# Kernel optimization log

Measured on AMD Instinct MI355X. Metric: run time of the kernel, lower is better.

## Reference

```python
import jax, jax.numpy as jnp
import numpy as np

D_MODEL = 1024
N_HEADS = 16
D_K = D_MODEL // N_HEADS


def setup_inputs() -> dict:
    key = jax.random.key(0)
    kx, kq, kk, kv, ko = jax.random.split(key, 5)
    scale = 1.0 / np.sqrt(D_MODEL)
    return {
        "x": jax.random.normal(kx, (2, 2048, D_MODEL), dtype=jnp.float32),
        "W_Q": jax.random.normal(kq, (D_MODEL, D_MODEL), dtype=jnp.float32) * scale,
        "W_K": jax.random.normal(kk, (D_MODEL, D_MODEL), dtype=jnp.float32) * scale,
        "W_V": jax.random.normal(kv, (D_MODEL, D_MODEL), dtype=jnp.float32) * scale,
        "W_O": jax.random.normal(ko, (D_MODEL, D_MODEL), dtype=jnp.float32) * scale,
    }


def reference(x, W_Q, W_K, W_V, W_O) -> jnp.ndarray:
    B, S, _ = x.shape
    # Projections; weights stored as (d_model, d_model), applied as x @ W (Linear weight transposed convention folded into init)
    def heads(w):
        return jnp.einsum('bsd,de->bse', x, w).reshape(B, S, N_HEADS, D_K).transpose(0, 2, 1, 3)
    Q, K, V = heads(W_Q), heads(W_K), heads(W_V)  # (B,H,S,d_k)
    scores = jnp.einsum('bhqd,bhkd->bhqk', Q, K) / jnp.sqrt(jnp.asarray(D_K, x.dtype))
    causal_mask = jnp.triu(jnp.ones((S, S), dtype=bool), k=1)  # True above diagonal
    scores = jnp.where(causal_mask[None, None], jnp.asarray(-jnp.inf, x.dtype), scores)
    attn = jax.nn.softmax(scores, axis=-1)
    out = jnp.einsum('bhqk,bhkd->bhqd', attn, V)  # (B,H,S,d_k)
    out = out.transpose(0, 2, 1, 3).reshape(B, S, N_HEADS * D_K)
    return jnp.einsum('bsd,de->bse', out, W_O)
```

## Files before the change

### kernel.cpp

```cpp
#include <hip/hip_runtime.h>

typedef unsigned short u16;
typedef unsigned int u32;
typedef __attribute__((ext_vector_type(8))) __bf16 bf16x8;
typedef __attribute__((ext_vector_type(2))) __bf16 bf16x2;
typedef __attribute__((ext_vector_type(4))) float f32x4;
typedef __attribute__((ext_vector_type(16))) float f32x16;
typedef __attribute__((ext_vector_type(4))) u32 u32x4;

__device__ inline u16 f2bf(float f) {
  unsigned u = __builtin_bit_cast(unsigned, f);
  u += 0x7FFFu + ((u >> 16) & 1u);
  return (u16)(u >> 16);
}

__device__ inline u32 packbf(float a, float b) {
  bf16x2 t;
  t[0] = (__bf16)a;
  t[1] = (__bf16)b;
  return __builtin_bit_cast(u32, t);
}

__device__ inline void async16(const void* g, void* l) {
  __builtin_amdgcn_global_load_lds((const __attribute__((address_space(1))) void*)g,
                                   (__attribute__((address_space(3))) void*)l, 16, 0, 0);
}

__global__ __launch_bounds__(256) void xconv(const float* __restrict__ x, u16* __restrict__ xb) {
  int i = blockIdx.x * 256 + threadIdx.x;
  float4 v = ((const float4*)x)[i];
  ushort4 r;
  r.x = f2bf(v.x); r.y = f2bf(v.y); r.z = f2bf(v.z); r.w = f2bf(v.w);
  ((ushort4*)xb)[i] = r;
}

__global__ __launch_bounds__(256) void wtrans4(const float* __restrict__ W0,
                                               const float* __restrict__ W1,
                                               const float* __restrict__ W2,
                                               const float* __restrict__ W3,
                                               u16* __restrict__ WtQKV,
                                               u16* __restrict__ WtO) {
  __shared__ u16 tile[32][33];
  const int z = blockIdx.z;
  const float* W = (z == 0) ? W0 : (z == 1) ? W1 : (z == 2) ? W2 : W3;
  u16* Wt = (z < 3) ? (WtQKV + (size_t)z * 1024 * 1024) : WtO;
  const float s = (z == 0) ? 0.18033688011112042f : 1.0f;
  const int e0 = blockIdx.x * 32;
  const int d0 = blockIdx.y * 32;
  const int tx = threadIdx.x & 31;
  const int ty = threadIdx.x >> 5;
#pragma unroll
  for (int i = ty; i < 32; i += 8)
    tile[i][tx] = f2bf(W[(size_t)(d0 + i) * 1024 + e0 + tx] * s);
  __syncthreads();
#pragma unroll
  for (int i = ty; i < 32; i += 8)
    Wt[(size_t)(e0 + i) * 1024 + d0 + tx] = tile[tx][i];
}

__global__ __launch_bounds__(256) void vtrans(const u16* __restrict__ QKV, u16* __restrict__ Vtg) {
  __shared__ u16 t[32][66];
  const int tid = threadIdx.x;
  const int s0 = blockIdx.x * 32, dg0 = blockIdx.y * 64, b = blockIdx.z;
  {
    const int i = tid >> 3, c = (tid & 7) * 8;
    uint4 v = *(const uint4*)(QKV + (size_t)(b * 2048 + s0 + i) * 3072 + 2048 + dg0 + c);
    u16 tmp[8];
    *(uint4*)tmp = v;
#pragma unroll
    for (int e = 0; e < 8; ++e) t[i][c + e] = tmp[e];
  }
  __syncthreads();
  {
    const int r = tid >> 2, cg = (tid & 3) * 8;
    u16 tmp[8];
#pragma unroll
    for (int e = 0; e < 8; ++e) {
      const int x = cg + e;
      const int sx = (x & ~12) | ((x & 4) << 1) | ((x & 8) >> 1);
      tmp[e] = t[sx][r];
    }
    *(uint4*)(Vtg + (size_t)(b * 1024 + dg0 + r) * 2048 + s0 + cg) = *(uint4*)tmp;
  }
}

template <int OUT_BF16>
__global__ __launch_bounds__(256) void gemm_bt(const u16* __restrict__ A,
                                               const u16* __restrict__ Bt,
                                               void* __restrict__ Cp,
                                               int M, int N, int K) {
  __shared__ __align__(16) u16 As[128 * 32];
  __shared__ __align__(16) u16 Bs[128 * 32];
  const int tid = threadIdx.x;
  const int lane = tid & 63;
  const int wave = tid >> 6;
  const int lr = lane & 15;
  const int lk = (lane >> 4) * 8;
  const int wm = (wave >> 1) * 64;
  const int wn = (wave & 1) * 64;
  const int bm = blockIdx.x * 128;
  const int bn = blockIdx.y * 128;
  const int srow = lane >> 2;
  const int scol = (lane & 3) * 8;

  f32x4 acc[4][4] = {};

  for (int k0 = 0; k0 < K; k0 += 32) {
#pragma unroll
    for (int r = 0; r < 2; ++r) {
      const int chunk = r * 4 + wave;
      const int row = chunk * 16 + srow;
      async16(A + (size_t)(bm + row) * K + k0 + scol, &As[chunk * 512 + lane * 8]);
      async16(Bt + (size_t)(bn + row) * K + k0 + scol, &Bs[chunk * 512 + lane * 8]);
    }
    __syncthreads();
    bf16x8 a[4], b[4];
#pragma unroll
    for (int i = 0; i < 4; ++i) {
      a[i] = *(const bf16x8*)&As[(wm + i * 16 + lr) * 32 + lk];
      b[i] = *(const bf16x8*)&Bs[(wn + i * 16 + lr) * 32 + lk];
    }
#pragma unroll
    for (int mi = 0; mi < 4; ++mi)
#pragma unroll
      for (int ni = 0; ni < 4; ++ni)
        acc[mi][ni] = __builtin_amdgcn_mfma_f32_16x16x32_bf16(a[mi], b[ni], acc[mi][ni], 0, 0, 0);
    __syncthreads();
  }

#pragma unroll
  for (int mi = 0; mi < 4; ++mi) {
#pragma unroll
    for (int ni = 0; ni < 4; ++ni) {
      const int col = bn + wn + ni * 16 + lr;
#pragma unroll
      for (int j = 0; j < 4; ++j) {
        const int row = bm + wm + mi * 16 + (lane >> 4) * 4 + j;
        if (OUT_BF16)
          ((u16*)Cp)[(size_t)row * N + col] = f2bf(acc[mi][ni][j]);
        else
          ((float*)Cp)[(size_t)row * N + col] = acc[mi][ni][j];
      }
    }
  }
}

__global__ __launch_bounds__(256, 2) void attn_kernel(const u16* __restrict__ QKV,
                                                      const u16* __restrict__ Vtg,
                                                      u16* __restrict__ Opart,
                                                      float* __restrict__ Lpart) {
  constexpr int S = 2048, LD = 3072;
  constexpr float MFIX = 12.0f;
  __shared__ __align__(16) u16 Ks[2][64 * 64];
  __shared__ __align__(16) u16 Vs[2][64 * 64];

  const int g = 7 - (blockIdx.x >> 1);
  const int c = blockIdx.x & 1;
  const int bh = blockIdx.y;
  const int b = bh >> 4, h = bh & 15;
  const int tid = threadIdx.x, lane = tid & 63, w = tid >> 6;
  const int l31 = lane & 31, lh = lane >> 5;

  const int qbase = g * 256 + w * 64;
  const int ktlast = 4 * g + w;
  const int ktbeg = c * (2 * g + 2);
  const int ktend = (c + 1) * (2 * g + 2);

  bf16x8 qf[2][4];
#pragma unroll
  for (int qh = 0; qh < 2; ++qh) {
    const u16* qrow = QKV + (size_t)(b * S + qbase + qh * 32 + l31) * LD + h * 64;
#pragma unroll
    for (int cc = 0; cc < 4; ++cc) qf[qh][cc] = *(const bf16x8*)(qrow + cc * 16 + lh * 8);
  }

  const int c0 = tid, c1 = tid + 256;
  const int r0 = c0 >> 3, x0 = ((c0 & 7) ^ (r0 & 7)) << 3;
  const int r1 = c1 >> 3, x1 = ((c1 & 7) ^ (r1 & 7)) << 3;
  const u16* Kbase = QKV + (size_t)b * S * LD + 1024 + h * 64;
  const u16* Vbase = Vtg + (size_t)bh * 64 * 2048;

#define STAGE(buf, kt_)                                                          \
  do {                                                                           \
    async16(Kbase + (size_t)((kt_)*64 + r0) * LD + x0, &Ks[buf][c0 * 8]);        \
    async16(Kbase + (size_t)((kt_)*64 + r1) * LD + x1, &Ks[buf][c1 * 8]);        \
    async16(Vbase + (size_t)r0 * 2048 + (kt_)*64 + x0, &Vs[buf][c0 * 8]);        \
    async16(Vbase + (size_t)r1 * 2048 + (kt_)*64 + x1, &Vs[buf][c1 * 8]);        \
  } while (0)

  f32x16 o00 = {}, o01 = {}, o10 = {}, o11 = {};
  float l0 = 0.f, l1 = 0.f;

#define TREE16(dst, arr)                                                         \
  do {                                                                           \
    float v_[16];                                                                \
    _Pragma("unroll") for (int r_ = 0; r_ < 16; ++r_) v_[r_] = (arr)[r_];        \
    _Pragma("unroll") for (int s_ = 8; s_ >= 1; s_ >>= 1)                        \
      _Pragma("unroll") for (int r_ = 0; r_ < s_; ++r_) v_[r_] += v_[r_ + s_];   \
    dst += v_[0];                                                                \
  } while (0)

#define MAKE_PA(pa, pk, q4)                                                      \
  bf16x8 pa;                                                                     \
  {                                                                              \
    u32x4 wv_;                                                                   \
    wv_[0] = (pk)[(q4) + 0];                                                     \
    wv_[1] = (pk)[(q4) + 1];                                                     \
    wv_[2] = (pk)[(q4) + 2];                                                     \
    wv_[3] = (pk)[(q4) + 3];                                                     \
    pa = __builtin_bit_cast(bf16x8, wv_);                                        \
  }

  STAGE(0, ktbeg);

  int cur = 0;
  for (int kt = ktbeg; kt < ktend; ++kt) {
    if (kt + 1 < ktend) {
      STAGE(cur ^ 1, kt + 1);
      asm volatile("s_waitcnt vmcnt(4)" ::: "memory");
    } else {
      asm volatile("s_waitcnt vmcnt(0)" ::: "memory");
    }
    __builtin_amdgcn_s_barrier();
    __builtin_amdgcn_sched_barrier(0);

    const bool active = (kt <= ktlast);
    if (active) {
      const bool full = (kt < ktlast);
      const u16* ks = Ks[cur];
      const u16* vs = Vs[cur];

      f32x16 t00 = {}, t10 = {}, t01 = {}, t11 = {};
      __builtin_amdgcn_s_setprio(1);
#pragma unroll
      for (int cc = 0; cc < 4; ++cc) {
        const int ci = 2 * cc + lh;
        const bf16x8 kf0 = *(const bf16x8*)&ks[l31 * 64 + ((ci ^ (l31 & 7)) << 3)];
        const bf16x8 kf1 = *(const bf16x8*)&ks[(32 + l31) * 64 + ((ci ^ (l31 & 7)) << 3)];
        t00 = __builtin_amdgcn_mfma_f32_32x32x16_bf16(kf0, qf[0][cc], t00, 0, 0, 0);
        t01 = __builtin_amdgcn_mfma_f32_32x32x16_bf16(kf0, qf[1][cc], t01, 0, 0, 0);
        if (full) t10 = __builtin_amdgcn_mfma_f32_32x32x16_bf16(kf1, qf[0][cc], t10, 0, 0, 0);
        t11 = __builtin_amdgcn_mfma_f32_32x32x16_bf16(kf1, qf[1][cc], t11, 0, 0, 0);
      }
      __builtin_amdgcn_s_setprio(0);

      if (!full) {
#pragma unroll
        for (int r = 0; r < 16; ++r) {
          const int ko = (r & 3) + 8 * (r >> 2) + 4 * lh;
          if (ko > l31) { t00[r] = -3e38f; t11[r] = -3e38f; }
        }
      }

      u32 pk0[8], pk1[8];

#pragma unroll
      for (int r = 0; r < 16; ++r) t00[r] = exp2f(t00[r] - MFIX);
#pragma unroll
      for (int r = 0; r < 16; ++r) t01[r] = exp2f(t01[r] - MFIX);
      TREE16(l0, t00);
      TREE16(l1, t01);
#pragma unroll
      for (int j = 0; j < 8; ++j) {
        pk0[j] = packbf(t00[2 * j], t00[2 * j + 1]);
        pk1[j] = packbf(t01[2 * j], t01[2 * j + 1]);
      }
      __builtin_amdgcn_s_setprio(1);
#pragma unroll
      for (int kc = 0; kc < 2; ++kc) {
        const int q4 = kc * 4;
        MAKE_PA(pa0, pk0, q4)
        MAKE_PA(pa1, pk1, q4)
        const int ci = 2 * kc + lh;
        const bf16x8 vd0 = *(const bf16x8*)&vs[l31 * 64 + ((ci ^ (l31 & 7)) << 3)];
        const bf16x8 vd1 = *(const bf16x8*)&vs[(32 + l31) * 64 + ((ci ^ (l31 & 7)) << 3)];
        o00 = __builtin_amdgcn_mfma_f32_32x32x16_bf16(pa0, vd0, o00, 0, 0, 0);
        o01 = __builtin_amdgcn_mfma_f32_32x32x16_bf16(pa0, vd1, o01, 0, 0, 0);
        o10 = __builtin_amdgcn_mfma_f32_32x32x16_bf16(pa1, vd0, o10, 0, 0, 0);
        o11 = __builtin_amdgcn_mfma_f32_32x32x16_bf16(pa1, vd1, o11, 0, 0, 0);
      }
      __builtin_amdgcn_s_setprio(0);

      if (full) {
#pragma unroll
        for (int r = 0; r < 16; ++r) t10[r] = exp2f(t10[r] - MFIX);
        TREE16(l0, t10);
#pragma unroll
        for (int j = 0; j < 8; ++j) pk0[j] = packbf(t10[2 * j], t10[2 * j + 1]);
      }
#pragma unroll
      for (int r = 0; r < 16; ++r) t11[r] = exp2f(t11[r] - MFIX);
      TREE16(l1, t11);
#pragma unroll
      for (int j = 0; j < 8; ++j) pk1[j] = packbf(t11[2 * j], t11[2 * j + 1]);

      __builtin_amdgcn_s_setprio(1);
#pragma unroll
      for (int kc = 0; kc < 2; ++kc) {
        const int q4 = kc * 4;
        MAKE_PA(pa1, pk1, q4)
        const int ci = 2 * (kc + 2) + lh;
        const bf16x8 vd0 = *(const bf16x8*)&vs[l31 * 64 + ((ci ^ (l31 & 7)) << 3)];
        const bf16x8 vd1 = *(const bf16x8*)&vs[(32 + l31) * 64 + ((ci ^ (l31 & 7)) << 3)];
        if (full) {
          MAKE_PA(pa0, pk0, q4)
          o00 = __builtin_amdgcn_mfma_f32_32x32x16_bf16(pa0, vd0, o00, 0, 0, 0);
          o01 = __builtin_amdgcn_mfma_f32_32x32x16_bf16(pa0, vd1, o01, 0, 0, 0);
        }
        o10 = __builtin_amdgcn_mfma_f32_32x32x16_bf16(pa1, vd0, o10, 0, 0, 0);
        o11 = __builtin_amdgcn_mfma_f32_32x32x16_bf16(pa1, vd1, o11, 0, 0, 0);
      }
      __builtin_amdgcn_s_setprio(0);
    }

    asm volatile("s_waitcnt lgkmcnt(0)" ::: "memory");
    __builtin_amdgcn_s_barrier();
    cur ^= 1;
  }
#undef STAGE
#undef TREE16
#undef MAKE_PA

  const float l0t = l0 + __shfl_xor(l0, 32);
  const float l1t = l1 + __shfl_xor(l1, 32);
  u16* Oc = Opart + (size_t)c * 4096 * 1024;
#pragma unroll
  for (int r = 0; r < 16; ++r) {
    const int qo = (r & 3) + 8 * (r >> 2) + 4 * lh;
    u16* p0 = Oc + (size_t)(b * S + qbase + qo) * 1024 + h * 64 + l31;
    u16* p1 = p0 + (size_t)32 * 1024;
    p0[0] = f2bf(o00[r]);
    p0[32] = f2bf(o01[r]);
    p1[0] = f2bf(o10[r]);
    p1[32] = f2bf(o11[r]);
  }
  if (lh == 0) {
    Lpart[(size_t)c * 4096 * 16 + (size_t)(b * S + qbase + l31) * 16 + h] = l0t;
    Lpart[(size_t)c * 4096 * 16 + (size_t)(b * S + qbase + 32 + l31) * 16 + h] = l1t;
  }
}

__global__ __launch_bounds__(256) void combine(const u16* __restrict__ Opart,
                                               const float* __restrict__ Lpart,
                                               u16* __restrict__ Obuf) {
  const int i = blockIdx.x * 256 + threadIdx.x;
  const int row = i >> 7;
  const int cw = (i & 127) * 8;
  const int h = cw >> 6;
  const float l = Lpart[(size_t)row * 16 + h] + Lpart[(size_t)4096 * 16 + (size_t)row * 16 + h];
  const float inv = 1.0f / l;
  const bf16x8 a = *(const bf16x8*)(Opart + (size_t)row * 1024 + cw);
  const bf16x8 bq = *(const bf16x8*)(Opart + (size_t)4096 * 1024 + (size_t)row * 1024 + cw);
  u16 out[8];
#pragma unroll
  for (int j = 0; j < 8; ++j) out[j] = f2bf(((float)a[j] + (float)bq[j]) * inv);
  *(uint4*)(Obuf + (size_t)row * 1024 + cw) = *(uint4*)out;
}

extern "C" void kernel_launch(void* const* d_in, const int* in_sizes, int n_in,
                              void* d_out, int out_size, void* d_ws, size_t ws_size,
                              hipStream_t stream) {
  const float* x  = (const float*)d_in[0];
  const float* WQ = (const float*)d_in[1];
  const float* WK = (const float*)d_in[2];
  const float* WV = (const float*)d_in[3];
  const float* WO = (const float*)d_in[4];
  float* out = (float*)d_out;

  u16* xb    = (u16*)d_ws;
  u16* WtQKV = xb + (size_t)4096 * 1024;
  u16* WtO   = WtQKV + (size_t)3072 * 1024;
  u16* QKV   = WtO + (size_t)1024 * 1024;
  u16* Obuf  = QKV + (size_t)4096 * 3072;
  u16* Vtg   = Obuf + (size_t)4096 * 1024;
  u16* Opart = Vtg + (size_t)2048 * 2048;
  float* Lpart = (float*)(Opart + (size_t)2 * 4096 * 1024);

  xconv<<<4096, 256, 0, stream>>>(x, xb);
  wtrans4<<<dim3(32, 32, 4), 256, 0, stream>>>(WQ, WK, WV, WO, WtQKV, WtO);

  gemm_bt<1><<<dim3(32, 24), 256, 0, stream>>>(xb, WtQKV, QKV, 4096, 3072, 1024);
  vtrans<<<dim3(64, 16, 2), 256, 0, stream>>>(QKV, Vtg);
  attn_kernel<<<dim3(16, 32), 256, 0, stream>>>(QKV, Vtg, Opart, Lpart);
  combine<<<2048, 256, 0, stream>>>(Opart, Lpart, Obuf);
  gemm_bt<0><<<dim3(32, 8), 256, 0, stream>>>(Obuf, WtO, out, 4096, 1024, 1024);
}
```

Before: 140.6 us.

## Use 128-key attention tiles and merge input-conversion launches into one prep kernel

The attention kernel now stages 128-key K/V tiles per iteration instead of 64, halving the number of barrier and wait steps per block. Each tile is processed as four 32-key sub-blocks with per-wave causal masking on the diagonal. Separately, the x conversion and the weight transposes are fused into a single launch using an extra grid z-slice. Larger tiles double LDS use per block, which may lower occupancy under the two-blocks-per-CU launch bound, and they coarsen the split of work on the causal diagonal.

```diff
diff --git a/kernel.cpp b/kernel.cpp
--- a/kernel.cpp
+++ b/kernel.cpp
@@ -26,22 +26,27 @@
                                    (__attribute__((address_space(3))) void*)l, 16, 0, 0);
 }
 
-__global__ __launch_bounds__(256) void xconv(const float* __restrict__ x, u16* __restrict__ xb) {
-  int i = blockIdx.x * 256 + threadIdx.x;
-  float4 v = ((const float4*)x)[i];
-  ushort4 r;
-  r.x = f2bf(v.x); r.y = f2bf(v.y); r.z = f2bf(v.z); r.w = f2bf(v.w);
-  ((ushort4*)xb)[i] = r;
-}
-
-__global__ __launch_bounds__(256) void wtrans4(const float* __restrict__ W0,
-                                               const float* __restrict__ W1,
-                                               const float* __restrict__ W2,
-                                               const float* __restrict__ W3,
-                                               u16* __restrict__ WtQKV,
-                                               u16* __restrict__ WtO) {
+__global__ __launch_bounds__(256) void prep(const float* __restrict__ x, u16* __restrict__ xb,
+                                            const float* __restrict__ W0,
+                                            const float* __restrict__ W1,
+                                            const float* __restrict__ W2,
+                                            const float* __restrict__ W3,
+                                            u16* __restrict__ WtQKV,
+                                            u16* __restrict__ WtO) {
+  const int z = blockIdx.z;
+  if (z == 4) {
+    const int base = (blockIdx.y * 32 + blockIdx.x) * 4 * 256 + threadIdx.x;
+#pragma unroll
+    for (int it = 0; it < 4; ++it) {
+      const int i = base + it * 256;
+      float4 v = ((const float4*)x)[i];
+      ushort4 r;
+      r.x = f2bf(v.x); r.y = f2bf(v.y); r.z = f2bf(v.z); r.w = f2bf(v.w);
+      ((ushort4*)xb)[i] = r;
+    }
+    return;
+  }
   __shared__ u16 tile[32][33];
-  const int z = blockIdx.z;
   const float* W = (z == 0) ? W0 : (z == 1) ? W1 : (z == 2) ? W2 : W3;
   u16* Wt = (z < 3) ? (WtQKV + (size_t)z * 1024 * 1024) : WtO;
   const float s = (z == 0) ? 0.18033688011112042f : 1.0f;
@@ -151,8 +156,8 @@
                                                       float* __restrict__ Lpart) {
   constexpr int S = 2048, LD = 3072;
   constexpr float MFIX = 12.0f;
-  __shared__ __align__(16) u16 Ks[2][64 * 64];
-  __shared__ __align__(16) u16 Vs[2][64 * 64];
+  __shared__ __align__(16) u16 Ks[2][128 * 64];
+  __shared__ __align__(16) u16 Vs[2][64 * 128];
 
   const int g = 7 - (blockIdx.x >> 1);
   const int c = blockIdx.x & 1;
@@ -162,9 +167,10 @@
   const int l31 = lane & 31, lh = lane >> 5;
 
   const int qbase = g * 256 + w * 64;
-  const int ktlast = 4 * g + w;
-  const int ktbeg = c * (2 * g + 2);
-  const int ktend = (c + 1) * (2 * g + 2);
+  const int ktlast = 2 * g + (w >> 1);
+  const int qblk = (w & 1) * 2;
+  const int ktbeg = c * (g + 1);
+  const int ktend = (c + 1) * (g + 1);
 
   bf16x8 qf[2][4];
 #pragma unroll
@@ -174,18 +180,23 @@
     for (int cc = 0; cc < 4; ++cc) qf[qh][cc] = *(const bf16x8*)(qrow + cc * 16 + lh * 8);
   }
 
-  const int c0 = tid, c1 = tid + 256;
-  const int r0 = c0 >> 3, x0 = ((c0 & 7) ^ (r0 & 7)) << 3;
-  const int r1 = c1 >> 3, x1 = ((c1 & 7) ^ (r1 & 7)) << 3;
   const u16* Kbase = QKV + (size_t)b * S * LD + 1024 + h * 64;
   const u16* Vbase = Vtg + (size_t)bh * 64 * 2048;
 
-#define STAGE(buf, kt_)                                                          \
-  do {                                                                           \
-    async16(Kbase + (size_t)((kt_)*64 + r0) * LD + x0, &Ks[buf][c0 * 8]);        \
-    async16(Kbase + (size_t)((kt_)*64 + r1) * LD + x1, &Ks[buf][c1 * 8]);        \
-    async16(Vbase + (size_t)r0 * 2048 + (kt_)*64 + x0, &Vs[buf][c0 * 8]);        \
-    async16(Vbase + (size_t)r1 * 2048 + (kt_)*64 + x1, &Vs[buf][c1 * 8]);        \
+#define STAGE(buf, kt_)                                                                 \
+  do {                                                                                  \
+    _Pragma("unroll") for (int i_ = 0; i_ < 4; ++i_) {                                  \
+      const int ch = tid + 256 * i_;                                                    \
+      const int kr = ch >> 3, kc = ch & 7;                                              \
+      async16(Kbase + (size_t)((kt_)*128 + kr) * LD + ((kc ^ (kr & 7)) << 3),           \
+              &Ks[buf][ch * 8]);                                                        \
+    }                                                                                   \
+    _Pragma("unroll") for (int i_ = 0; i_ < 4; ++i_) {                                  \
+      const int ch = tid + 256 * i_;                                                    \
+      const int vd = ch >> 4, vc = ch & 15;                                             \
+      async16(Vbase + (size_t)vd * 2048 + (kt_)*128 + ((vc ^ (vd & 7)) << 3),           \
+              &Vs[buf][ch * 8]);                                                        \
+    }                                                                                   \
   } while (0)
 
   f32x16 o00 = {}, o01 = {}, o10 = {}, o11 = {};
@@ -217,100 +228,77 @@
   for (int kt = ktbeg; kt < ktend; ++kt) {
     if (kt + 1 < ktend) {
       STAGE(cur ^ 1, kt + 1);
-      asm volatile("s_waitcnt vmcnt(4)" ::: "memory");
+      asm volatile("s_waitcnt vmcnt(8)" ::: "memory");
     } else {
       asm volatile("s_waitcnt vmcnt(0)" ::: "memory");
     }
     __builtin_amdgcn_s_barrier();
     __builtin_amdgcn_sched_barrier(0);
 
-    const bool active = (kt <= ktlast);
-    if (active) {
-      const bool full = (kt < ktlast);
+    if (kt <= ktlast) {
+      const bool dtile = (kt == ktlast);
       const u16* ks = Ks[cur];
       const u16* vs = Vs[cur];
 
-      f32x16 t00 = {}, t10 = {}, t01 = {}, t11 = {};
-      __builtin_amdgcn_s_setprio(1);
-#pragma unroll
-      for (int cc = 0; cc < 4; ++cc) {
-        const int ci = 2 * cc + lh;
-        const bf16x8 kf0 = *(const bf16x8*)&ks[l31 * 64 + ((ci ^ (l31 & 7)) << 3)];
-        const bf16x8 kf1 = *(const bf16x8*)&ks[(32 + l31) * 64 + ((ci ^ (l31 & 7)) << 3)];
-        t00 = __builtin_amdgcn_mfma_f32_32x32x16_bf16(kf0, qf[0][cc], t00, 0, 0, 0);
-        t01 = __builtin_amdgcn_mfma_f32_32x32x16_bf16(kf0, qf[1][cc], t01, 0, 0, 0);
-        if (full) t10 = __builtin_amdgcn_mfma_f32_32x32x16_bf16(kf1, qf[0][cc], t10, 0, 0, 0);
-        t11 = __builtin_amdgcn_mfma_f32_32x32x16_bf16(kf1, qf[1][cc], t11, 0, 0, 0);
+#pragma unroll
+      for (int kq = 0; kq < 4; ++kq) {
+        const bool en0 = !dtile || (kq <= qblk);
+        const bool en1 = !dtile || (kq <= qblk + 1);
+        const bool dg0 = dtile && (kq == qblk);
+        const bool dg1 = dtile && (kq == qblk + 1);
+        if (!en1) break;
+
+        f32x16 t0 = {}, t1 = {};
+        __builtin_amdgcn_s_setprio(1);
+#pragma unroll
+        for (int cc = 0; cc < 4; ++cc) {
+          const int ci = 2 * cc + lh;
+          const bf16x8 kf = *(const bf16x8*)&ks[(kq * 32 + l31) * 64 + ((ci ^ (l31 & 7)) << 3)];
+          if (en0) t0 = __builtin_amdgcn_mfma_f32_32x32x16_bf16(kf, qf[0][cc], t0, 0, 0, 0);
+          t1 = __builtin_amdgcn_mfma_f32_32x32x16_bf16(kf, qf[1][cc], t1, 0, 0, 0);
+        }
+        __builtin_amdgcn_s_setprio(0);
+
+        if (dg0 || dg1) {
+#pragma unroll
+          for (int r = 0; r < 16; ++r) {
+            const int ko = (r & 3) + 8 * (r >> 2) + 4 * lh;
+            if (dg0 && ko > l31) t0[r] = -3e38f;
+            if (dg1 && ko > l31) t1[r] = -3e38f;
+          }
+        }
+
+        u32 pk0[8], pk1[8];
+        if (en0) {
+#pragma unroll
+          for (int r = 0; r < 16; ++r) t0[r] = exp2f(t0[r] - MFIX);
+          TREE16(l0, t0);
+#pragma unroll
+          for (int j = 0; j < 8; ++j) pk0[j] = packbf(t0[2 * j], t0[2 * j + 1]);
+        }
+#pragma unroll
+        for (int r = 0; r < 16; ++r) t1[r] = exp2f(t1[r] - MFIX);
+        TREE16(l1, t1);
+#pragma unroll
+        for (int j = 0; j < 8; ++j) pk1[j] = packbf(t1[2 * j], t1[2 * j + 1]);
+
+        __builtin_amdgcn_s_setprio(1);
+#pragma unroll
+        for (int kc = 0; kc < 2; ++kc) {
+          const int ci = kq * 4 + 2 * kc + lh;
+          const bf16x8 vd0 = *(const bf16x8*)&vs[l31 * 128 + ((ci ^ (l31 & 7)) << 3)];
+          const bf16x8 vd1 = *(const bf16x8*)&vs[(32 + l31) * 128 + ((ci ^ (l31 & 7)) << 3)];
+          MAKE_PA(pa1, pk1, kc * 4)
+          if (en0) {
+            MAKE_PA(pa0, pk0, kc * 4)
+            o00 = __builtin_amdgcn_mfma_f32_32x32x16_bf16(pa0, vd0, o00, 0, 0, 0);
+            o01 = __builtin_amdgcn_mfma_f32_32x32x16_bf16(pa0, vd1, o01, 0, 0, 0);
+          }
+          o10 = __builtin_amdgcn_mfma_f32_32x32x16_bf16(pa1, vd0, o10, 0, 0, 0);
+          o11 = __builtin_amdgcn_mfma_f32_32x32x16_bf16(pa1, vd1, o11, 0, 0, 0);
+        }
+        __builtin_amdgcn_s_setprio(0);
       }
-      __builtin_amdgcn_s_setprio(0);
-
-      if (!full) {
-#pragma unroll
-        for (int r = 0; r < 16; ++r) {
-          const int ko = (r & 3) + 8 * (r >> 2) + 4 * lh;
-          if (ko > l31) { t00[r] = -3e38f; t11[r] = -3e38f; }
-        }
-      }
-
-      u32 pk0[8], pk1[8];
-
-#pragma unroll
-      for (int r = 0; r < 16; ++r) t00[r] = exp2f(t00[r] - MFIX);
-#pragma unroll
-      for (int r = 0; r < 16; ++r) t01[r] = exp2f(t01[r] - MFIX);
-      TREE16(l0, t00);
-      TREE16(l1, t01);
-#pragma unroll
-      for (int j = 0; j < 8; ++j) {
-        pk0[j] = packbf(t00[2 * j], t00[2 * j + 1]);
-        pk1[j] = packbf(t01[2 * j], t01[2 * j + 1]);
-      }
-      __builtin_amdgcn_s_setprio(1);
-#pragma unroll
-      for (int kc = 0; kc < 2; ++kc) {
-        const int q4 = kc * 4;
-        MAKE_PA(pa0, pk0, q4)
-        MAKE_PA(pa1, pk1, q4)
-        const int ci = 2 * kc + lh;
-        const bf16x8 vd0 = *(const bf16x8*)&vs[l31 * 64 + ((ci ^ (l31 & 7)) << 3)];
-        const bf16x8 vd1 = *(const bf16x8*)&vs[(32 + l31) * 64 + ((ci ^ (l31 & 7)) << 3)];
-        o00 = __builtin_amdgcn_mfma_f32_32x32x16_bf16(pa0, vd0, o00, 0, 0, 0);
-        o01 = __builtin_amdgcn_mfma_f32_32x32x16_bf16(pa0, vd1, o01, 0, 0, 0);
-        o10 = __builtin_amdgcn_mfma_f32_32x32x16_bf16(pa1, vd0, o10, 0, 0, 0);
-        o11 = __builtin_amdgcn_mfma_f32_32x32x16_bf16(pa1, vd1, o11, 0, 0, 0);
-      }
-      __builtin_amdgcn_s_setprio(0);
-
-      if (full) {
-#pragma unroll
-        for (int r = 0; r < 16; ++r) t10[r] = exp2f(t10[r] - MFIX);
-        TREE16(l0, t10);
-#pragma unroll
-        for (int j = 0; j < 8; ++j) pk0[j] = packbf(t10[2 * j], t10[2 * j + 1]);
-      }
-#pragma unroll
-      for (int r = 0; r < 16; ++r) t11[r] = exp2f(t11[r] - MFIX);
-      TREE16(l1, t11);
-#pragma unroll
-      for (int j = 0; j < 8; ++j) pk1[j] = packbf(t11[2 * j], t11[2 * j + 1]);
-
-      __builtin_amdgcn_s_setprio(1);
-#pragma unroll
-      for (int kc = 0; kc < 2; ++kc) {
-        const int q4 = kc * 4;
-        MAKE_PA(pa1, pk1, q4)
-        const int ci = 2 * (kc + 2) + lh;
-        const bf16x8 vd0 = *(const bf16x8*)&vs[l31 * 64 + ((ci ^ (l31 & 7)) << 3)];
-        const bf16x8 vd1 = *(const bf16x8*)&vs[(32 + l31) * 64 + ((ci ^ (l31 & 7)) << 3)];
-        if (full) {
-          MAKE_PA(pa0, pk0, q4)
-          o00 = __builtin_amdgcn_mfma_f32_32x32x16_bf16(pa0, vd0, o00, 0, 0, 0);
-          o01 = __builtin_amdgcn_mfma_f32_32x32x16_bf16(pa0, vd1, o01, 0, 0, 0);
-        }
-        o10 = __builtin_amdgcn_mfma_f32_32x32x16_bf16(pa1, vd0, o10, 0, 0, 0);
-        o11 = __builtin_amdgcn_mfma_f32_32x32x16_bf16(pa1, vd1, o11, 0, 0, 0);
-      }
-      __builtin_amdgcn_s_setprio(0);
     }
 
     asm volatile("s_waitcnt lgkmcnt(0)" ::: "memory");
@@ -376,8 +364,7 @@
   u16* Opart = Vtg + (size_t)2048 * 2048;
   float* Lpart = (float*)(Opart + (size_t)2 * 4096 * 1024);
 
-  xconv<<<4096, 256, 0, stream>>>(x, xb);
-  wtrans4<<<dim3(32, 32, 4), 256, 0, stream>>>(WQ, WK, WV, WO, WtQKV, WtO);
+  prep<<<dim3(32, 32, 5), 256, 0, stream>>>(x, xb, WQ, WK, WV, WO, WtQKV, WtO);
 
   gemm_bt<1><<<dim3(32, 24), 256, 0, stream>>>(xb, WtQKV, QKV, 4096, 3072, 1024);
   vtrans<<<dim3(64, 16, 2), 256, 0, stream>>>(QKV, Vtg);
```

New measurement: 139.7 us. Within noise of the previous version (-0.7%).

## Fuse prep kernels, fold V transpose into QKV GEMM, remap block order

Applied to the files above, without the earlier changes.

Merges the x-to-bf16 conversion and the weight transpose into one launch, using an extra grid z-slice for the conversion. The separate V-transpose kernel is removed: the QKV GEMM epilogue writes permuted, transposed V directly into Vtg. Block-index swizzles are added to the GEMM and attention kernels to spread consecutive blocks across chiplets/XCDs. This removes two launches and a read-back pass over V, at the cost of extra strided 8-byte stores in the GEMM epilogue.

```diff
diff --git a/kernel.cpp b/kernel.cpp
--- a/kernel.cpp
+++ b/kernel.cpp
@@ -26,22 +26,27 @@
                                    (__attribute__((address_space(3))) void*)l, 16, 0, 0);
 }
 
-__global__ __launch_bounds__(256) void xconv(const float* __restrict__ x, u16* __restrict__ xb) {
-  int i = blockIdx.x * 256 + threadIdx.x;
-  float4 v = ((const float4*)x)[i];
-  ushort4 r;
-  r.x = f2bf(v.x); r.y = f2bf(v.y); r.z = f2bf(v.z); r.w = f2bf(v.w);
-  ((ushort4*)xb)[i] = r;
-}
-
-__global__ __launch_bounds__(256) void wtrans4(const float* __restrict__ W0,
-                                               const float* __restrict__ W1,
-                                               const float* __restrict__ W2,
-                                               const float* __restrict__ W3,
-                                               u16* __restrict__ WtQKV,
-                                               u16* __restrict__ WtO) {
+__global__ __launch_bounds__(256) void prep(const float* __restrict__ x, u16* __restrict__ xb,
+                                            const float* __restrict__ W0,
+                                            const float* __restrict__ W1,
+                                            const float* __restrict__ W2,
+                                            const float* __restrict__ W3,
+                                            u16* __restrict__ WtQKV,
+                                            u16* __restrict__ WtO) {
+  const int z = blockIdx.z;
+  if (z == 4) {
+    const int base = (blockIdx.y * 32 + blockIdx.x) * 4 * 256 + threadIdx.x;
+#pragma unroll
+    for (int it = 0; it < 4; ++it) {
+      const int i = base + it * 256;
+      float4 v = ((const float4*)x)[i];
+      ushort4 r;
+      r.x = f2bf(v.x); r.y = f2bf(v.y); r.z = f2bf(v.z); r.w = f2bf(v.w);
+      ((ushort4*)xb)[i] = r;
+    }
+    return;
+  }
   __shared__ u16 tile[32][33];
-  const int z = blockIdx.z;
   const float* W = (z == 0) ? W0 : (z == 1) ? W1 : (z == 2) ? W2 : W3;
   u16* Wt = (z < 3) ? (WtQKV + (size_t)z * 1024 * 1024) : WtO;
   const float s = (z == 0) ? 0.18033688011112042f : 1.0f;
@@ -58,36 +63,11 @@
     Wt[(size_t)(e0 + i) * 1024 + d0 + tx] = tile[tx][i];
 }
 
-__global__ __launch_bounds__(256) void vtrans(const u16* __restrict__ QKV, u16* __restrict__ Vtg) {
-  __shared__ u16 t[32][66];
-  const int tid = threadIdx.x;
-  const int s0 = blockIdx.x * 32, dg0 = blockIdx.y * 64, b = blockIdx.z;
-  {
-    const int i = tid >> 3, c = (tid & 7) * 8;
-    uint4 v = *(const uint4*)(QKV + (size_t)(b * 2048 + s0 + i) * 3072 + 2048 + dg0 + c);
-    u16 tmp[8];
-    *(uint4*)tmp = v;
-#pragma unroll
-    for (int e = 0; e < 8; ++e) t[i][c + e] = tmp[e];
-  }
-  __syncthreads();
-  {
-    const int r = tid >> 2, cg = (tid & 3) * 8;
-    u16 tmp[8];
-#pragma unroll
-    for (int e = 0; e < 8; ++e) {
-      const int x = cg + e;
-      const int sx = (x & ~12) | ((x & 4) << 1) | ((x & 8) >> 1);
-      tmp[e] = t[sx][r];
-    }
-    *(uint4*)(Vtg + (size_t)(b * 1024 + dg0 + r) * 2048 + s0 + cg) = *(uint4*)tmp;
-  }
-}
-
-template <int OUT_BF16>
+template <int OUT_BF16, int FUSE_V>
 __global__ __launch_bounds__(256) void gemm_bt(const u16* __restrict__ A,
                                                const u16* __restrict__ Bt,
                                                void* __restrict__ Cp,
+                                               u16* __restrict__ Vtg,
                                                int M, int N, int K) {
   __shared__ __align__(16) u16 As[128 * 32];
   __shared__ __align__(16) u16 Bs[128 * 32];
@@ -98,8 +78,13 @@
   const int lk = (lane >> 4) * 8;
   const int wm = (wave >> 1) * 64;
   const int wn = (wave & 1) * 64;
-  const int bm = blockIdx.x * 128;
-  const int bn = blockIdx.y * 128;
+
+  const int flat = blockIdx.y * gridDim.x + blockIdx.x;
+  const int chunk = (gridDim.x * gridDim.y) >> 3;
+  const int nf = (flat & 7) * chunk + (flat >> 3);
+  const int bm = (nf % gridDim.x) * 128;
+  const int bn = (nf / gridDim.x) * 128;
+
   const int srow = lane >> 2;
   const int scol = (lane & 3) * 8;
 
@@ -108,10 +93,10 @@
   for (int k0 = 0; k0 < K; k0 += 32) {
 #pragma unroll
     for (int r = 0; r < 2; ++r) {
-      const int chunk = r * 4 + wave;
-      const int row = chunk * 16 + srow;
-      async16(A + (size_t)(bm + row) * K + k0 + scol, &As[chunk * 512 + lane * 8]);
-      async16(Bt + (size_t)(bn + row) * K + k0 + scol, &Bs[chunk * 512 + lane * 8]);
+      const int chnk = r * 4 + wave;
+      const int row = chnk * 16 + srow;
+      async16(A + (size_t)(bm + row) * K + k0 + scol, &As[chnk * 512 + lane * 8]);
+      async16(Bt + (size_t)(bn + row) * K + k0 + scol, &Bs[chnk * 512 + lane * 8]);
     }
     __syncthreads();
     bf16x8 a[4], b[4];
@@ -130,16 +115,27 @@
 
 #pragma unroll
   for (int mi = 0; mi < 4; ++mi) {
+    const int row = bm + wm + mi * 16 + (lane >> 4) * 4;
 #pragma unroll
     for (int ni = 0; ni < 4; ++ni) {
       const int col = bn + wn + ni * 16 + lr;
 #pragma unroll
       for (int j = 0; j < 4; ++j) {
-        const int row = bm + wm + mi * 16 + (lane >> 4) * 4 + j;
         if (OUT_BF16)
-          ((u16*)Cp)[(size_t)row * N + col] = f2bf(acc[mi][ni][j]);
+          ((u16*)Cp)[(size_t)(row + j) * N + col] = f2bf(acc[mi][ni][j]);
         else
-          ((float*)Cp)[(size_t)row * N + col] = acc[mi][ni][j];
+          ((float*)Cp)[(size_t)(row + j) * N + col] = acc[mi][ni][j];
+      }
+      if (FUSE_V && col >= 2048) {
+        const int bloc = row >> 11;
+        const int s = row & 2047;
+        const int sp = (s & ~12) | ((s & 4) << 1) | ((s & 8) >> 1);
+        ushort4 v4;
+        v4.x = f2bf(acc[mi][ni][0]);
+        v4.y = f2bf(acc[mi][ni][1]);
+        v4.z = f2bf(acc[mi][ni][2]);
+        v4.w = f2bf(acc[mi][ni][3]);
+        *(ushort4*)(Vtg + (size_t)(bloc * 1024 + (col - 2048)) * 2048 + sp) = v4;
       }
     }
   }
@@ -154,9 +150,13 @@
   __shared__ __align__(16) u16 Ks[2][64 * 64];
   __shared__ __align__(16) u16 Vs[2][64 * 64];
 
-  const int g = 7 - (blockIdx.x >> 1);
-  const int c = blockIdx.x & 1;
-  const int bh = blockIdx.y;
+  const int flat = blockIdx.y * 16 + blockIdx.x;
+  const int nf = (flat & 7) * 64 + (flat >> 3);
+  const int xi = nf & 15;
+  const int bh = nf >> 4;
+
+  const int g = 7 - (xi >> 1);
+  const int c = xi & 1;
   const int b = bh >> 4, h = bh & 15;
   const int tid = threadIdx.x, lane = tid & 63, w = tid >> 6;
   const int l31 = lane & 31, lh = lane >> 5;
@@ -376,12 +376,10 @@
   u16* Opart = Vtg + (size_t)2048 * 2048;
   float* Lpart = (float*)(Opart + (size_t)2 * 4096 * 1024);
 
-  xconv<<<4096, 256, 0, stream>>>(x, xb);
-  wtrans4<<<dim3(32, 32, 4), 256, 0, stream>>>(WQ, WK, WV, WO, WtQKV, WtO);
-
-  gemm_bt<1><<<dim3(32, 24), 256, 0, stream>>>(xb, WtQKV, QKV, 4096, 3072, 1024);
-  vtrans<<<dim3(64, 16, 2), 256, 0, stream>>>(QKV, Vtg);
+  prep<<<dim3(32, 32, 5), 256, 0, stream>>>(x, xb, WQ, WK, WV, WO, WtQKV, WtO);
+
+  gemm_bt<1, 1><<<dim3(32, 24), 256, 0, stream>>>(xb, WtQKV, QKV, Vtg, 4096, 3072, 1024);
   attn_kernel<<<dim3(16, 32), 256, 0, stream>>>(QKV, Vtg, Opart, Lpart);
   combine<<<2048, 256, 0, stream>>>(Opart, Lpart, Obuf);
-  gemm_bt<0><<<dim3(32, 8), 256, 0, stream>>>(Obuf, WtO, out, 4096, 1024, 1024);
-}
+  gemm_bt<0, 0><<<dim3(32, 8), 256, 0, stream>>>(Obuf, WtO, out, nullptr, 4096, 1024, 1024);
+}
```

Result: no change. 138.2 us, median of 3 (-1.7%).
